# Kernel tuning notes

Hardware: AMD Instinct MI355X
Metric: run time of the kernel (lower is better)

## Reference

```python
import jax, jax.numpy as jnp
import numpy as np

TWO_PI = 2.0 * np.pi


def setup_inputs() -> dict:
    key = jax.random.key(0)
    k1, k2, k3, k4 = jax.random.split(key, 4)
    N, H, W, B = 1024, 256, 256, 64
    pred = jax.random.uniform(k1, (N,), dtype=jnp.float32)
    mu = jax.random.uniform(k2, (N, 2), dtype=jnp.float32)              # centers in [0,1]
    sigma = jax.random.uniform(k3, (N, 2), dtype=jnp.float32) * 0.25 + 0.05  # widths in [0.05,0.30]
    nodes = jnp.concatenate([mu, sigma], axis=1)                         # [N,4]
    batch_list = jax.random.randint(k4, (N,), 0, B, dtype=jnp.int64)
    return {"pred": pred, "nodes": nodes, "batch_list": batch_list,
            "h": H, "w": W, "batch_num": B}


def reference(pred, nodes, batch_list, h, w, batch_num):
    # Normalized grid, identical to torch.arange(num)*step + start
    xs = jnp.linspace(0.0, 1.0, w, dtype=pred.dtype)   # [w]
    ys = jnp.linspace(0.0, 1.0, h, dtype=pred.dtype)   # [h]
    x_t = xs[None, :]                                   # broadcasts to [h,w]
    y_t = ys[:, None]

    mu_x = nodes[:, 0][:, None, None]
    mu_y = nodes[:, 1][:, None, None]
    sx = nodes[:, 2][:, None, None]
    sy = nodes[:, 3][:, None, None]

    # [N,h,w] per-node gaussian (epsilon = 0 in the original module)
    g = (1.0 / (TWO_PI * sx * sy)) * jnp.exp(
        -((x_t[None] - mu_x) ** 2 / (2.0 * sx ** 2)
          + (y_t[None] - mu_y) ** 2 / (2.0 * sy ** 2)))

    # normalize each node map by its max, scale by pred[i]
    g = g / jnp.max(g, axis=(1, 2), keepdims=True) * pred[:, None, None]

    # scatter-add into per-batch maps
    maps = jax.ops.segment_sum(g, batch_list, num_segments=batch_num)   # [B,h,w]
    return maps[:, None, :, :]                                          # [B,1,h,w]
```

## Files before the change

### kernel.cpp

```cpp
#include <hip/hip_runtime.h>
#include <math.h>

#define HCONST 256
#define WCONST 256
#define NMAX   1024
#define TILE_Y 16
#define TILES  (HCONST / TILE_Y)

__global__ __launch_bounds__(WCONST) void fused_kernel(
    const float* __restrict__ pred,
    const float* __restrict__ nodes,
    const int*   __restrict__ batch_list,
    int N,
    float* __restrict__ out)
{
    const int b  = blockIdx.x / TILES;
    const int ty = blockIdx.x % TILES;
    const int y0 = ty * TILE_Y;
    const int x  = threadIdx.x;

    __shared__ int s_idx[NMAX];
    __shared__ int s_cnt;
    if (x == 0) s_cnt = 0;
    __syncthreads();
    for (int n = x; n < N; n += WCONST) {
        if (batch_list[n] == b) {
            int p = atomicAdd(&s_cnt, 1);
            s_idx[p] = n;
        }
    }
    __syncthreads();
    const int cnt = s_cnt;

    float acc[TILE_Y];
#pragma unroll
    for (int yy = 0; yy < TILE_Y; ++yy) acc[yy] = 0.0f;

    const float step  = 1.0f / 255.0f;
    const float xs    = x * step;
    const float ylane = (y0 + (x & (TILE_Y - 1))) * step;

    for (int g = 0; g < cnt; ++g) {
        const int n = s_idx[g];
        const float4 nd = ((const float4*)nodes)[n];
        const float pr = pred[n];

        const float ax = 1.0f / (2.0f * nd.z * nd.z);
        const float ay = 1.0f / (2.0f * nd.w * nd.w);

        const float nix = fminf(fmaxf(roundf(nd.x * 255.0f), 0.0f), 255.0f);
        const float niy = fminf(fmaxf(roundf(nd.y * 255.0f), 0.0f), 255.0f);
        const float dxm = nix * step - nd.x;
        const float dym = niy * step - nd.y;

        const float dx = xs - nd.x;
        const float fx = __expf(-ax * (dx * dx - dxm * dxm)) * pr;

        const float dy  = ylane - nd.y;
        const float fyv = __expf(-ay * (dy * dy - dym * dym));

#pragma unroll
        for (int yy = 0; yy < TILE_Y; ++yy)
            acc[yy] = fmaf(__shfl(fyv, yy, TILE_Y), fx, acc[yy]);
    }

    float* o = out + ((size_t)b * HCONST + y0) * WCONST + x;
#pragma unroll
    for (int yy = 0; yy < TILE_Y; ++yy)
        o[yy * WCONST] = acc[yy];
}

extern "C" void kernel_launch(void* const* d_in, const int* in_sizes, int n_in,
                              void* d_out, int out_size, void* d_ws, size_t ws_size,
                              hipStream_t stream) {
    const float* pred       = (const float*)d_in[0];
    const float* nodes      = (const float*)d_in[1];
    const int*   batch_list = (const int*)d_in[2];

    const int N = in_sizes[0];
    const int B = out_size / (HCONST * WCONST);

    float* out = (float*)d_out;

    fused_kernel<<<B * TILES, WCONST, 0, stream>>>(pred, nodes, batch_list, N, out);
}
```

Before: 87.35 us.

## Precompute per-node row factors in shared memory and tile 32 rows by two columns

Each block now covers 32 rows, and each thread computes 2 columns by 16 rows. Per-node x parameters and y-factors (with pred folded in) are precomputed chunk-wise into shared memory, replacing per-node redundant exp computation and 16 cross-lane shuffles with float4 LDS broadcast reads. This cuts redundant transcendental work and shuffle overhead. In exchange, the grid has half as many blocks (512), and each chunk adds extra barriers.

```diff
diff --git a/kernel.cpp b/kernel.cpp
--- a/kernel.cpp
+++ b/kernel.cpp
@@ -3,11 +3,11 @@
 
 #define HCONST 256
 #define WCONST 256
-#define NMAX   1024
-#define TILE_Y 16
-#define TILES  (HCONST / TILE_Y)
+#define ROWS   32
+#define TILES  (HCONST / ROWS)
+#define CHUNK  64
 
-__global__ __launch_bounds__(WCONST) void fused_kernel(
+__global__ __launch_bounds__(256) void fused_kernel(
     const float* __restrict__ pred,
     const float* __restrict__ nodes,
     const int*   __restrict__ batch_list,
@@ -16,14 +16,19 @@
 {
     const int b  = blockIdx.x / TILES;
     const int ty = blockIdx.x % TILES;
-    const int y0 = ty * TILE_Y;
-    const int x  = threadIdx.x;
+    const int y0 = ty * ROWS;
+    const int t  = threadIdx.x;
+    const int xi   = t & 127;
+    const int half = t >> 7;
 
-    __shared__ int s_idx[NMAX];
-    __shared__ int s_cnt;
-    if (x == 0) s_cnt = 0;
+    __shared__ int    s_idx[1024];
+    __shared__ int    s_cnt;
+    __shared__ float4 s_prm[CHUNK];
+    __shared__ float  s_fy[CHUNK][ROWS];
+
+    if (t == 0) s_cnt = 0;
     __syncthreads();
-    for (int n = x; n < N; n += WCONST) {
+    for (int n = t; n < N; n += 256) {
         if (batch_list[n] == b) {
             int p = atomicAdd(&s_cnt, 1);
             s_idx[p] = n;
@@ -32,42 +37,67 @@
     __syncthreads();
     const int cnt = s_cnt;
 
-    float acc[TILE_Y];
+    const float step = 1.0f / 255.0f;
+    const float x0s = (2 * xi)     * step;
+    const float x1s = (2 * xi + 1) * step;
+
+    float2 acc[16];
 #pragma unroll
-    for (int yy = 0; yy < TILE_Y; ++yy) acc[yy] = 0.0f;
+    for (int r = 0; r < 16; ++r) acc[r] = make_float2(0.0f, 0.0f);
 
-    const float step  = 1.0f / 255.0f;
-    const float xs    = x * step;
-    const float ylane = (y0 + (x & (TILE_Y - 1))) * step;
+    for (int c0 = 0; c0 < cnt; c0 += CHUNK) {
+        const int cc = min(CHUNK, cnt - c0);
 
-    for (int g = 0; g < cnt; ++g) {
-        const int n = s_idx[g];
-        const float4 nd = ((const float4*)nodes)[n];
-        const float pr = pred[n];
+        for (int p = t; p < cc; p += 256) {
+            const int n = s_idx[c0 + p];
+            const float4 nd = ((const float4*)nodes)[n];
+            const float ax = 1.0f / (2.0f * nd.z * nd.z);
+            float ni = roundf(nd.x * 255.0f);
+            ni = fminf(fmaxf(ni, 0.0f), 255.0f);
+            const float dxm = ni * step - nd.x;
+            s_prm[p] = make_float4(nd.x, ax, ax * dxm * dxm, 0.0f);
+        }
+        for (int it = t; it < cc * ROWS; it += 256) {
+            const int g  = it >> 5;
+            const int yy = it & 31;
+            const int n  = s_idx[c0 + g];
+            const float4 nd = ((const float4*)nodes)[n];
+            const float ay = 1.0f / (2.0f * nd.w * nd.w);
+            float ni = roundf(nd.y * 255.0f);
+            ni = fminf(fmaxf(ni, 0.0f), 255.0f);
+            const float dym = ni * step - nd.y;
+            const float dy  = (y0 + yy) * step - nd.y;
+            s_fy[g][yy] = pred[n] * __expf(ay * (dym * dym - dy * dy));
+        }
+        __syncthreads();
 
-        const float ax = 1.0f / (2.0f * nd.z * nd.z);
-        const float ay = 1.0f / (2.0f * nd.w * nd.w);
-
-        const float nix = fminf(fmaxf(roundf(nd.x * 255.0f), 0.0f), 255.0f);
-        const float niy = fminf(fmaxf(roundf(nd.y * 255.0f), 0.0f), 255.0f);
-        const float dxm = nix * step - nd.x;
-        const float dym = niy * step - nd.y;
-
-        const float dx = xs - nd.x;
-        const float fx = __expf(-ax * (dx * dx - dxm * dxm)) * pr;
-
-        const float dy  = ylane - nd.y;
-        const float fyv = __expf(-ay * (dy * dy - dym * dym));
-
+        for (int g = 0; g < cc; ++g) {
+            const float4 prm = s_prm[g];
+            const float dx0 = x0s - prm.x;
+            const float dx1 = x1s - prm.x;
+            const float e0 = __expf(prm.z - prm.y * dx0 * dx0);
+            const float e1 = __expf(prm.z - prm.y * dx1 * dx1);
+            const float4* fy4 = (const float4*)&s_fy[g][half * 16];
 #pragma unroll
-        for (int yy = 0; yy < TILE_Y; ++yy)
-            acc[yy] = fmaf(__shfl(fyv, yy, TILE_Y), fx, acc[yy]);
+            for (int k = 0; k < 4; ++k) {
+                const float4 f = fy4[k];
+                acc[k*4+0].x = fmaf(f.x, e0, acc[k*4+0].x);
+                acc[k*4+0].y = fmaf(f.x, e1, acc[k*4+0].y);
+                acc[k*4+1].x = fmaf(f.y, e0, acc[k*4+1].x);
+                acc[k*4+1].y = fmaf(f.y, e1, acc[k*4+1].y);
+                acc[k*4+2].x = fmaf(f.z, e0, acc[k*4+2].x);
+                acc[k*4+2].y = fmaf(f.z, e1, acc[k*4+2].y);
+                acc[k*4+3].x = fmaf(f.w, e0, acc[k*4+3].x);
+                acc[k*4+3].y = fmaf(f.w, e1, acc[k*4+3].y);
+            }
+        }
+        __syncthreads();
     }
 
-    float* o = out + ((size_t)b * HCONST + y0) * WCONST + x;
+    float* o = out + ((size_t)b * HCONST + y0 + half * 16) * WCONST + 2 * xi;
 #pragma unroll
-    for (int yy = 0; yy < TILE_Y; ++yy)
-        o[yy * WCONST] = acc[yy];
+    for (int r = 0; r < 16; ++r)
+        ((float2*)(o + (size_t)r * WCONST))[0] = acc[r];
 }
 
 extern "C" void kernel_launch(void* const* d_in, const int* in_sizes, int n_in,
@@ -82,5 +112,5 @@
 
     float* out = (float*)d_out;
 
-    fused_kernel<<<B * TILES, WCONST, 0, stream>>>(pred, nodes, batch_list, N, out);
+    fused_kernel<<<B * TILES, 256, 0, stream>>>(pred, nodes, batch_list, N, out);
 }
```

Result: faster. 74.12 us (-15.1%).
